# Performance work log

Measured on AMD Instinct MI355X. Metric: run time of the kernel, lower is better.

## Reference

```python
import jax, jax.numpy as jnp
import numpy as np

EPS = 1e-5

def _sage(x, src, dst, counts, w_msg, w_root, b, n_nodes):
    # mean-aggregate neighbor features (src -> dst), then linear
    msgs = x[src]                                             # [E, D]
    summed = jax.ops.segment_sum(msgs, dst, num_segments=n_nodes)
    mean = summed / counts                                    # [N, D]
    return mean @ w_msg + x @ w_root + b

def _layernorm(x, gamma, beta):
    mu = jnp.mean(x, axis=-1, keepdims=True)
    var = jnp.var(x, axis=-1, keepdims=True)
    return (x - mu) * jax.lax.rsqrt(var + EPS) * gamma + beta

def setup_inputs() -> dict:
    key = jax.random.key(0)
    N, E, D = 100000, 1600000, 128
    ks = jax.random.split(key, 20)
    z = jax.random.normal(ks[0], (N, D), dtype=jnp.float32)
    edge_index = jax.random.randint(ks[1], (2, E), 0, N, dtype=jnp.int32)
    def lin(k, din, dout):
        return jax.random.normal(k, (din, dout), dtype=jnp.float32) / np.sqrt(din)
    params = {
        'w_msg1': lin(ks[2], 128, 256), 'w_root1': lin(ks[3], 128, 256),
        'b1': jnp.zeros((256,), jnp.float32),
        'g1': jax.random.uniform(ks[4], (256,), jnp.float32, 0.9, 1.1),
        'beta1': jax.random.normal(ks[5], (256,), jnp.float32) * 0.05,
        'w_msg2': lin(ks[6], 256, 256), 'w_root2': lin(ks[7], 256, 256),
        'b2': jnp.zeros((256,), jnp.float32),
        'g2': jax.random.uniform(ks[8], (256,), jnp.float32, 0.9, 1.1),
        'beta2': jax.random.normal(ks[9], (256,), jnp.float32) * 0.05,
        'w_msg3': lin(ks[10], 256, 128), 'w_root3': lin(ks[11], 256, 128),
        'b3': jnp.zeros((128,), jnp.float32),
        'g3': jax.random.uniform(ks[12], (128,), jnp.float32, 0.9, 1.1),
        'beta3': jax.random.normal(ks[13], (128,), jnp.float32) * 0.05,
        'w_msg4': lin(ks[14], 128, 9), 'w_root4': lin(ks[15], 128, 9),
        'b4': jnp.zeros((9,), jnp.float32),
    }
    return {'z': z, 'edge_index': edge_index, **params}

def reference(z, edge_index,
              w_msg1, w_root1, b1, g1, beta1,
              w_msg2, w_root2, b2, g2, beta2,
              w_msg3, w_root3, b3, g3, beta3,
              w_msg4, w_root4, b4):
    N = z.shape[0]
    src, dst = edge_index[0], edge_index[1]
    counts = jax.ops.segment_sum(jnp.ones_like(dst, dtype=z.dtype), dst, num_segments=N)
    counts = jnp.maximum(counts, 1.0)[:, None]
    x = jax.nn.relu(_layernorm(_sage(z, src, dst, counts, w_msg1, w_root1, b1, N), g1, beta1))
    x = jax.nn.relu(_layernorm(_sage(x, src, dst, counts, w_msg2, w_root2, b2, N), g2, beta2))
    x = jax.nn.relu(_layernorm(_sage(x, src, dst, counts, w_msg3, w_root3, b3, N), g3, beta3))
    x = _sage(x, src, dst, counts, w_msg4, w_root4, b4, N)
    return x
```

## Files before the change

### kernel.cpp

```cpp
#include <hip/hip_runtime.h>
#include <hip/hip_bf16.h>


#define EPS 1e-5f

typedef unsigned short u16;
typedef short bf16x8_t __attribute__((ext_vector_type(8)));
typedef float f32x4_t __attribute__((ext_vector_type(4)));

__device__ inline unsigned int bfpack(float a, float b) {
    unsigned int ua = __builtin_bit_cast(unsigned int, a);
    unsigned int ub = __builtin_bit_cast(unsigned int, b);
    ua += 0x7fffu + ((ua >> 16) & 1u);
    ub += 0x7fffu + ((ub >> 16) & 1u);
    return (ua >> 16) | (ub & 0xffff0000u);
}

__device__ inline u16 bfr(float a) {
    unsigned int u = __builtin_bit_cast(unsigned int, a);
    u += 0x7fffu + ((u >> 16) & 1u);
    return (u16)(u >> 16);
}

__device__ inline float bf2f(u16 v) {
    unsigned int u = ((unsigned int)v) << 16;
    return __builtin_bit_cast(float, u);
}

__global__ __launch_bounds__(256) void zero_f4(float4* __restrict__ p, int n4) {
    int i = blockIdx.x * 256 + threadIdx.x;
    if (i < n4) p[i] = make_float4(0.f, 0.f, 0.f, 0.f);
}

__global__ __launch_bounds__(256) void cast_bf16(const float* __restrict__ x,
                                                 u16* __restrict__ y, int n4) {
    int i = blockIdx.x * 256 + threadIdx.x;
    if (i >= n4) return;
    float4 v = ((const float4*)x)[i];
    ((uint2*)y)[i] = make_uint2(bfpack(v.x, v.y), bfpack(v.z, v.w));
}

struct WtJobs {
    const float* W[6];
    u16* WT[6];
    int K[6], N[6];
};
__global__ __launch_bounds__(256) void transpose_cast6(WtJobs jobs) {
    int j = blockIdx.y;
    int idx = blockIdx.x * 256 + threadIdx.x;
    int K = jobs.K[j], Nn = jobs.N[j];
    if (idx >= K * Nn) return;
    int k = idx / Nn, n = idx - k * Nn;
    jobs.WT[j][(long)n * K + k] = bfr(jobs.W[j][idx]);
}

__global__ __launch_bounds__(256) void count_deg(const int* __restrict__ dst,
                                                 int* __restrict__ deg, int E) {
    int e = blockIdx.x * 256 + threadIdx.x;
    if (e < E) atomicAdd(&deg[dst[e]], 1);
}

__global__ __launch_bounds__(256) void partial_sums(const int* __restrict__ deg,
                                                    int* __restrict__ partials, int N) {
    __shared__ int lds[4];
    int tid = threadIdx.x;
    int base = blockIdx.x * 1024 + tid * 4;
    int s = 0;
    if (base + 3 < N) {
        int4 v = *(const int4*)(deg + base);
        s = v.x + v.y + v.z + v.w;
    } else {
        for (int i = 0; i < 4; ++i)
            if (base + i < N) s += deg[base + i];
    }
#pragma unroll
    for (int m = 32; m >= 1; m >>= 1) s += __shfl_xor(s, m);
    if ((tid & 63) == 0) lds[tid >> 6] = s;
    __syncthreads();
    if (tid == 0) partials[blockIdx.x] = lds[0] + lds[1] + lds[2] + lds[3];
}

__global__ __launch_bounds__(256) void scan_partials(int* __restrict__ partials, int nb) {
    __shared__ int lds[256];
    int tid = threadIdx.x;
    int v = (tid < nb) ? partials[tid] : 0;
    lds[tid] = v;
    __syncthreads();
    for (int off = 1; off < 256; off <<= 1) {
        int t = (tid >= off) ? lds[tid - off] : 0;
        __syncthreads();
        lds[tid] += t;
        __syncthreads();
    }
    if (tid < nb) partials[tid] = lds[tid] - v;
}

__global__ __launch_bounds__(256) void write_rowptr(const int* __restrict__ deg,
                                                    const int* __restrict__ partials,
                                                    int* __restrict__ rowptr,
                                                    int* __restrict__ cursor,
                                                    float* __restrict__ inv, int N, int E) {
    __shared__ int lds[256];
    int tid = threadIdx.x;
    int base = blockIdx.x * 1024 + tid * 4;
    int d[4];
    int s = 0;
#pragma unroll
    for (int i = 0; i < 4; ++i) {
        d[i] = (base + i < N) ? deg[base + i] : 0;
        s += d[i];
    }
    lds[tid] = s;
    __syncthreads();
    for (int off = 1; off < 256; off <<= 1) {
        int t = (tid >= off) ? lds[tid - off] : 0;
        __syncthreads();
        lds[tid] += t;
        __syncthreads();
    }
    int run = partials[blockIdx.x] + lds[tid] - s;
#pragma unroll
    for (int i = 0; i < 4; ++i) {
        int idx = base + i;
        if (idx < N) {
            rowptr[idx] = run;
            cursor[idx] = run;
            inv[idx] = 1.0f / fmaxf((float)d[i], 1.0f);
            run += d[i];
        }
    }
    if (blockIdx.x == 0 && tid == 0) rowptr[N] = E;
}

__global__ __launch_bounds__(256) void fill_csr_range(const int* __restrict__ src,
                                                      const int* __restrict__ dst,
                                                      int* __restrict__ cursor,
                                                      int* __restrict__ eidx, int E,
                                                      int lo, int bs) {
    int e = blockIdx.x * 256 + threadIdx.x;
    if (e >= E) return;
    int d = dst[e];
    if ((unsigned)(d - lo) < (unsigned)bs) {
        int p = atomicAdd(&cursor[d], 1);
        eidx[p] = src[e];
    }
}

__global__ __launch_bounds__(256) void gather_scale256(const u16* __restrict__ x,
                                                       const int* __restrict__ rowptr,
                                                       const int* __restrict__ eidx,
                                                       const float* __restrict__ inv,
                                                       u16* __restrict__ agg, int N) {
    int wave = threadIdx.x >> 6;
    int lane = threadIdx.x & 63;
    int row = blockIdx.x * 4 + wave;
    if (row >= N) return;
    int beg = rowptr[row], end = rowptr[row + 1];
    const ushort4* xv = (const ushort4*)x;
    float a0 = 0.f, a1 = 0.f, a2 = 0.f, a3 = 0.f;
    float c0 = 0.f, c1 = 0.f, c2 = 0.f, c3 = 0.f;
    int j = beg;
    for (; j + 1 < end; j += 2) {
        ushort4 v = xv[(long)eidx[j] * 64 + lane];
        ushort4 w = xv[(long)eidx[j + 1] * 64 + lane];
        a0 += bf2f(v.x); a1 += bf2f(v.y); a2 += bf2f(v.z); a3 += bf2f(v.w);
        c0 += bf2f(w.x); c1 += bf2f(w.y); c2 += bf2f(w.z); c3 += bf2f(w.w);
    }
    if (j < end) {
        ushort4 v = xv[(long)eidx[j] * 64 + lane];
        a0 += bf2f(v.x); a1 += bf2f(v.y); a2 += bf2f(v.z); a3 += bf2f(v.w);
    }
    float s = inv[row];
    a0 = (a0 + c0) * s; a1 = (a1 + c1) * s; a2 = (a2 + c2) * s; a3 = (a3 + c3) * s;
    ((uint2*)agg)[(long)row * 64 + lane] = make_uint2(bfpack(a0, a1), bfpack(a2, a3));
}

__global__ __launch_bounds__(256) void gather_scale128(const u16* __restrict__ x,
                                                       const int* __restrict__ rowptr,
                                                       const int* __restrict__ eidx,
                                                       const float* __restrict__ inv,
                                                       u16* __restrict__ agg, int N) {
    int half = threadIdx.x >> 5;
    int lane = threadIdx.x & 31;
    int row = blockIdx.x * 8 + half;
    if (row >= N) return;
    int beg = rowptr[row], end = rowptr[row + 1];
    const ushort4* xv = (const ushort4*)x;
    float a0 = 0.f, a1 = 0.f, a2 = 0.f, a3 = 0.f;
    float c0 = 0.f, c1 = 0.f, c2 = 0.f, c3 = 0.f;
    int j = beg;
    for (; j + 1 < end; j += 2) {
        ushort4 v = xv[(long)eidx[j] * 32 + lane];
        ushort4 w = xv[(long)eidx[j + 1] * 32 + lane];
        a0 += bf2f(v.x); a1 += bf2f(v.y); a2 += bf2f(v.z); a3 += bf2f(v.w);
        c0 += bf2f(w.x); c1 += bf2f(w.y); c2 += bf2f(w.z); c3 += bf2f(w.w);
    }
    if (j < end) {
        ushort4 v = xv[(long)eidx[j] * 32 + lane];
        a0 += bf2f(v.x); a1 += bf2f(v.y); a2 += bf2f(v.z); a3 += bf2f(v.w);
    }
    float s = inv[row];
    a0 = (a0 + c0) * s; a1 = (a1 + c1) * s; a2 = (a2 + c2) * s; a3 = (a3 + c3) * s;
    ((uint2*)agg)[(long)row * 32 + lane] = make_uint2(bfpack(a0, a1), bfpack(a2, a3));
}

__global__ __launch_bounds__(256) void gather_add_ln_relu128(const u16* __restrict__ y,
                                                             const int* __restrict__ rowptr,
                                                             const int* __restrict__ eidx,
                                                             const float* __restrict__ inv,
                                                             const u16* __restrict__ r,
                                                             const float* __restrict__ g,
                                                             const float* __restrict__ be,
                                                             u16* __restrict__ out, int N) {
    int half = threadIdx.x >> 5;
    int lane = threadIdx.x & 31;
    int row = blockIdx.x * 8 + half;
    if (row >= N) return;
    int beg = rowptr[row], end = rowptr[row + 1];
    const ushort4* xv = (const ushort4*)y;
    float a0 = 0.f, a1 = 0.f, a2 = 0.f, a3 = 0.f;
    float c0 = 0.f, c1 = 0.f, c2 = 0.f, c3 = 0.f;
    int j = beg;
    for (; j + 1 < end; j += 2) {
        ushort4 v = xv[(long)eidx[j] * 32 + lane];
        ushort4 w = xv[(long)eidx[j + 1] * 32 + lane];
        a0 += bf2f(v.x); a1 += bf2f(v.y); a2 += bf2f(v.z); a3 += bf2f(v.w);
        c0 += bf2f(w.x); c1 += bf2f(w.y); c2 += bf2f(w.z); c3 += bf2f(w.w);
    }
    if (j < end) {
        ushort4 v = xv[(long)eidx[j] * 32 + lane];
        a0 += bf2f(v.x); a1 += bf2f(v.y); a2 += bf2f(v.z); a3 += bf2f(v.w);
    }
    float iv = inv[row];
    ushort4 rr = ((const ushort4*)r)[(long)row * 32 + lane];
    float v0 = (a0 + c0) * iv + bf2f(rr.x);
    float v1 = (a1 + c1) * iv + bf2f(rr.y);
    float v2 = (a2 + c2) * iv + bf2f(rr.z);
    float v3 = (a3 + c3) * iv + bf2f(rr.w);
    float s = v0 + v1 + v2 + v3;
    float ss = v0 * v0 + v1 * v1 + v2 * v2 + v3 * v3;
#pragma unroll
    for (int m = 16; m >= 1; m >>= 1) {
        s += __shfl_xor(s, m);
        ss += __shfl_xor(ss, m);
    }
    float mean = s / 128.f;
    float var = ss / 128.f - mean * mean;
    float rs = rsqrtf(var + EPS);
    int col = lane * 4;
    v0 = fmaxf((v0 - mean) * rs * g[col + 0] + be[col + 0], 0.f);
    v1 = fmaxf((v1 - mean) * rs * g[col + 1] + be[col + 1], 0.f);
    v2 = fmaxf((v2 - mean) * rs * g[col + 2] + be[col + 2], 0.f);
    v3 = fmaxf((v3 - mean) * rs * g[col + 3] + be[col + 3], 0.f);
    ((uint2*)out)[(long)row * 32 + lane] = make_uint2(bfpack(v0, v1), bfpack(v2, v3));
}

__global__ __launch_bounds__(256) void gather9_final(const u16* __restrict__ y,
                                                     const int* __restrict__ rowptr,
                                                     const int* __restrict__ eidx,
                                                     const float* __restrict__ inv,
                                                     const float* __restrict__ r,
                                                     float* __restrict__ out, int N) {
    int idx = blockIdx.x * 256 + threadIdx.x;
    int row = idx >> 4;
    int c = idx & 15;
    if (row >= N || c >= 9) return;
    int beg = rowptr[row], end = rowptr[row + 1];
    float a = 0.f;
    for (int j = beg; j < end; ++j) a += bf2f(y[(long)eidx[j] * 9 + c]);
    out[(long)row * 9 + c] = a * inv[row] + r[(long)row * 9 + c];
}

__global__ __launch_bounds__(256) void mfma_gemm_wide_ln(const u16* A1,
                                                         const u16* __restrict__ A2,
                                                         const u16* __restrict__ WT1,
                                                         const u16* __restrict__ WT2,
                                                         const float* __restrict__ bias,
                                                         const float* __restrict__ g,
                                                         const float* __restrict__ be,
                                                         u16* out, int M, int K) {
    __shared__ __align__(16) u16 smem[64 * 260];
    u16* As = smem;
    u16* Ws = smem + 64 * 40;
    const int tid = threadIdx.x;
    const int bm = blockIdx.x * 64;
    const int l = tid & 63;
    const int w = tid >> 6;
    const int wr = (w & 1) * 32;
    const int wc = (w >> 1) * 128;
    const int ln15 = l & 15;
    const int quad = l >> 4;

    f32x4_t acc[2][8];
#pragma unroll
    for (int i = 0; i < 2; ++i)
#pragma unroll
        for (int j = 0; j < 8; ++j) acc[i][j] = (f32x4_t){0.f, 0.f, 0.f, 0.f};

    const int ar = tid >> 2;
    const int akh = (tid & 3) * 8;

    for (int pass = 0; pass < 2; ++pass) {
        const u16* A = pass ? A2 : A1;
        const u16* WT = pass ? WT2 : WT1;
        for (int k0 = 0; k0 < K; k0 += 32) {
            uint4 q0 = make_uint4(0, 0, 0, 0);
            int gr = bm + ar;
            if (gr < M) q0 = *(const uint4*)(A + (long)gr * K + k0 + akh);
            *(uint4*)(As + ar * 40 + akh) = q0;
            const u16* wp = WT + (long)tid * K + k0;
            *(uint4*)(Ws + tid * 40 + 0) = ((const uint4*)wp)[0];
            *(uint4*)(Ws + tid * 40 + 8) = ((const uint4*)wp)[1];
            *(uint4*)(Ws + tid * 40 + 16) = ((const uint4*)wp)[2];
            *(uint4*)(Ws + tid * 40 + 24) = ((const uint4*)wp)[3];
            __syncthreads();

            bf16x8_t a[2], b[8];
#pragma unroll
            for (int i = 0; i < 2; ++i)
                a[i] = *(const bf16x8_t*)(As + (wr + i * 16 + ln15) * 40 + quad * 8);
#pragma unroll
            for (int j = 0; j < 8; ++j)
                b[j] = *(const bf16x8_t*)(Ws + (wc + j * 16 + ln15) * 40 + quad * 8);
#pragma unroll
            for (int i = 0; i < 2; ++i)
#pragma unroll
                for (int j = 0; j < 8; ++j)
                    acc[i][j] = __builtin_amdgcn_mfma_f32_16x16x32_bf16(a[i], b[j], acc[i][j], 0, 0, 0);
            __syncthreads();
        }
    }

#pragma unroll
    for (int j = 0; j < 8; ++j) {
        int col = wc + j * 16 + ln15;
        float bv = bias[col];
#pragma unroll
        for (int i = 0; i < 2; ++i) {
            int row0 = wr + i * 16 + quad * 4;
            f32x4_t c = acc[i][j];
#pragma unroll
            for (int p = 0; p < 4; ++p) smem[(row0 + p) * 260 + col] = bfr(c[p] + bv);
        }
    }
    __syncthreads();

    float4 g4 = *(const float4*)&g[l * 4];
    float4 be4 = *(const float4*)&be[l * 4];
    for (int rr = 0; rr < 16; ++rr) {
        int lrow = w * 16 + rr;
        int grow = bm + lrow;
        if (grow >= M) break;
        ushort4 ld = *(const ushort4*)(smem + lrow * 260 + l * 4);
        float v0 = bf2f(ld.x), v1 = bf2f(ld.y), v2 = bf2f(ld.z), v3 = bf2f(ld.w);
        float s = v0 + v1 + v2 + v3;
        float ss = v0 * v0 + v1 * v1 + v2 * v2 + v3 * v3;
#pragma unroll
        for (int m = 32; m >= 1; m >>= 1) {
            s += __shfl_xor(s, m);
            ss += __shfl_xor(ss, m);
        }
        float mean = s / 256.f;
        float var = ss / 256.f - mean * mean;
        float rs = rsqrtf(var + EPS);
        v0 = fmaxf((v0 - mean) * rs * g4.x + be4.x, 0.f);
        v1 = fmaxf((v1 - mean) * rs * g4.y + be4.y, 0.f);
        v2 = fmaxf((v2 - mean) * rs * g4.z + be4.z, 0.f);
        v3 = fmaxf((v3 - mean) * rs * g4.w + be4.w, 0.f);
        ((uint2*)out)[(long)grow * 64 + l] = make_uint2(bfpack(v0, v1), bfpack(v2, v3));
    }
}

__global__ __launch_bounds__(256) void mfma_gemm_dual(const u16* __restrict__ A,
                                                      const u16* __restrict__ WTa,
                                                      const u16* __restrict__ WTb,
                                                      const float* __restrict__ biasb,
                                                      u16* __restrict__ outa,
                                                      u16* __restrict__ outb, int M, int K) {
    __shared__ u16 As[128 * 40];
    __shared__ u16 Ws[128 * 40];
    const u16* WT = blockIdx.y ? WTb : WTa;
    u16* out = blockIdx.y ? outb : outa;
    const float* bias = blockIdx.y ? biasb : nullptr;
    const int tid = threadIdx.x;
    const int bm = blockIdx.x * 128;
    const int l = tid & 63;
    const int w = tid >> 6;
    const int wr = (w & 1) * 64;
    const int wc = (w >> 1) * 64;
    const int ln15 = l & 15;
    const int quad = l >> 4;

    f32x4_t acc[4][4];
#pragma unroll
    for (int i = 0; i < 4; ++i)
#pragma unroll
        for (int j = 0; j < 4; ++j) acc[i][j] = (f32x4_t){0.f, 0.f, 0.f, 0.f};

    const int sr = tid >> 1;
    const int kh = (tid & 1) * 16;

    for (int k0 = 0; k0 < K; k0 += 32) {
        uint4 q0 = make_uint4(0, 0, 0, 0), q1 = make_uint4(0, 0, 0, 0);
        int gr = bm + sr;
        if (gr < M) {
            const u16* ap = A + (long)gr * K + k0 + kh;
            q0 = ((const uint4*)ap)[0];
            q1 = ((const uint4*)ap)[1];
        }
        *(uint4*)(As + sr * 40 + kh) = q0;
        *(uint4*)(As + sr * 40 + kh + 8) = q1;
        const u16* wp = WT + (long)sr * K + k0 + kh;
        *(uint4*)(Ws + sr * 40 + kh) = ((const uint4*)wp)[0];
        *(uint4*)(Ws + sr * 40 + kh + 8) = ((const uint4*)wp)[1];
        __syncthreads();

        bf16x8_t a[4], b[4];
#pragma unroll
        for (int i = 0; i < 4; ++i)
            a[i] = *(const bf16x8_t*)(As + (wr + i * 16 + ln15) * 40 + quad * 8);
#pragma unroll
        for (int j = 0; j < 4; ++j)
            b[j] = *(const bf16x8_t*)(Ws + (wc + j * 16 + ln15) * 40 + quad * 8);
#pragma unroll
        for (int i = 0; i < 4; ++i)
#pragma unroll
            for (int j = 0; j < 4; ++j)
                acc[i][j] = __builtin_amdgcn_mfma_f32_16x16x32_bf16(a[i], b[j], acc[i][j], 0, 0, 0);
        __syncthreads();
    }

#pragma unroll
    for (int j = 0; j < 4; ++j) {
        int col = wc + j * 16 + ln15;
        float bv = bias ? bias[col] : 0.f;
#pragma unroll
        for (int i = 0; i < 4; ++i) {
            int row0 = bm + wr + i * 16 + quad * 4;
            f32x4_t c = acc[i][j];
#pragma unroll
            for (int p = 0; p < 4; ++p) {
                int row = row0 + p;
                if (row < M) out[(long)row * 128 + col] = bfr(c[p] + bv);
            }
        }
    }
}

__global__ __launch_bounds__(320) void gemm4_bf(const u16* __restrict__ x,
                                                const float* __restrict__ wm,
                                                const float* __restrict__ wrt,
                                                const float* __restrict__ b,
                                                u16* __restrict__ y, float* __restrict__ r,
                                                int M) {
    __shared__ float xs[16][132];
    __shared__ float ws[128][20];
    int tid = threadIdx.x;
    int m0 = blockIdx.x * 16;
    for (int idx = tid; idx < 16 * 128; idx += 320) {
        int rr = idx >> 7, kk = idx & 127;
        int gm = m0 + rr;
        xs[rr][kk] = (gm < M) ? bf2f(x[(long)gm * 128 + kk]) : 0.f;
    }
    for (int idx = tid; idx < 128 * 18; idx += 320) {
        int kk = idx / 18, cc = idx % 18;
        ws[kk][cc] = (cc < 9) ? wm[kk * 9 + cc] : wrt[kk * 9 + cc - 9];
    }
    __syncthreads();
    if (tid < 288) {
        int rr = tid / 18, cc = tid % 18;
        float acc = 0.f;
#pragma unroll 8
        for (int kk = 0; kk < 128; ++kk) acc += xs[rr][kk] * ws[kk][cc];
        int gm = m0 + rr;
        if (gm < M) {
            if (cc < 9) y[(long)gm * 9 + cc] = bfr(acc);
            else r[(long)gm * 9 + cc - 9] = acc + b[cc - 9];
        }
    }
}

static inline int cdiv(long a, long b) { return (int)((a + b - 1) / b); }

extern "C" void kernel_launch(void* const* d_in, const int* in_sizes, int n_in,
                              void* d_out, int out_size, void* d_ws, size_t ws_size,
                              hipStream_t stream) {
    const int N = in_sizes[0] / 128;
    const int E = in_sizes[1] / 2;

    const float* z = (const float*)d_in[0];
    const int* ei = (const int*)d_in[1];
    const int* src = ei;
    const int* dstp = ei + E;
    const float* wm1 = (const float*)d_in[2];
    const float* wr1 = (const float*)d_in[3];
    const float* b1 = (const float*)d_in[4];
    const float* g1 = (const float*)d_in[5];
    const float* be1 = (const float*)d_in[6];
    const float* wm2 = (const float*)d_in[7];
    const float* wr2 = (const float*)d_in[8];
    const float* b2 = (const float*)d_in[9];
    const float* g2 = (const float*)d_in[10];
    const float* be2 = (const float*)d_in[11];
    const float* wm3 = (const float*)d_in[12];
    const float* wr3 = (const float*)d_in[13];
    const float* b3 = (const float*)d_in[14];
    const float* g3 = (const float*)d_in[15];
    const float* be3 = (const float*)d_in[16];
    const float* wm4 = (const float*)d_in[17];
    const float* wr4 = (const float*)d_in[18];
    const float* b4 = (const float*)d_in[19];
    float* out = (float*)d_out;

    u16* aggh2 = (u16*)d_ws;
    u16* h1b = aggh2 + (size_t)N * 256;
    u16* zb = h1b + (size_t)N * 256;
    u16* agg1 = zb + (size_t)N * 128;
    float* inv = (float*)(agg1 + (size_t)N * 128);
    int* deg = (int*)(inv + N);
    int* rowptr = deg + N + 4;
    int* cursor = rowptr + N + 4;
    int* partials = cursor + N + 4;
    int* eidx = partials + 256;
    u16* wt1m = (u16*)(eidx + E);
    u16* wt1r = wt1m + 256 * 128;
    u16* wt2m = wt1r + 256 * 128;
    u16* wt2r = wt2m + 256 * 256;
    u16* wt3m = wt2r + 256 * 256;
    u16* wt3r = wt3m + 128 * 256;

    u16* y3b = agg1;
    u16* r3b = zb;
    u16* h3b = h1b;
    u16* y4 = aggh2;
    float* r4 = (float*)(aggh2 + (size_t)N * 16);

    const int nscan = cdiv(N, 1024);

    cast_bf16<<<cdiv((long)N * 32, 256), 256, 0, stream>>>(z, zb, N * 32);
    zero_f4<<<cdiv(N, 1024), 256, 0, stream>>>((float4*)deg, cdiv(N, 4));
    count_deg<<<cdiv(E, 256), 256, 0, stream>>>(dstp, deg, E);
    partial_sums<<<nscan, 256, 0, stream>>>(deg, partials, N);
    scan_partials<<<1, 256, 0, stream>>>(partials, nscan);
    write_rowptr<<<nscan, 256, 0, stream>>>(deg, partials, rowptr, cursor, inv, N, E);
    {
        const int P = 8;
        int bs = cdiv(N, P);
        for (int b = 0; b < P; ++b)
            fill_csr_range<<<cdiv(E, 256), 256, 0, stream>>>(src, dstp, cursor, eidx, E,
                                                             b * bs, bs);
    }
    {
        WtJobs jobs;
        jobs.W[0] = wm1; jobs.WT[0] = wt1m; jobs.K[0] = 128; jobs.N[0] = 256;
        jobs.W[1] = wr1; jobs.WT[1] = wt1r; jobs.K[1] = 128; jobs.N[1] = 256;
        jobs.W[2] = wm2; jobs.WT[2] = wt2m; jobs.K[2] = 256; jobs.N[2] = 256;
        jobs.W[3] = wr2; jobs.WT[3] = wt2r; jobs.K[3] = 256; jobs.N[3] = 256;
        jobs.W[4] = wm3; jobs.WT[4] = wt3m; jobs.K[4] = 256; jobs.N[4] = 128;
        jobs.W[5] = wr3; jobs.WT[5] = wt3r; jobs.K[5] = 256; jobs.N[5] = 128;
        dim3 g(256, 6);
        transpose_cast6<<<g, 256, 0, stream>>>(jobs);
    }

    gather_scale128<<<cdiv(N, 8), 256, 0, stream>>>(zb, rowptr, eidx, inv, agg1, N);
    mfma_gemm_wide_ln<<<cdiv(N, 64), 256, 0, stream>>>(agg1, zb, wt1m, wt1r, b1, g1, be1,
                                                       h1b, N, 128);

    gather_scale256<<<cdiv(N, 4), 256, 0, stream>>>(h1b, rowptr, eidx, inv, aggh2, N);
    mfma_gemm_wide_ln<<<cdiv(N, 64), 256, 0, stream>>>(aggh2, h1b, wt2m, wt2r, b2, g2, be2,
                                                       aggh2, N, 256);

    {
        dim3 g(cdiv(N, 128), 2);
        mfma_gemm_dual<<<g, 256, 0, stream>>>(aggh2, wt3m, wt3r, b3, y3b, r3b, N, 256);
    }
    gather_add_ln_relu128<<<cdiv(N, 8), 256, 0, stream>>>(y3b, rowptr, eidx, inv, r3b, g3,
                                                          be3, h3b, N);

    gemm4_bf<<<cdiv(N, 16), 320, 0, stream>>>(h3b, wm4, wr4, b4, y4, r4, N);
    gather9_final<<<cdiv((long)N * 16, 256), 256, 0, stream>>>(y4, rowptr, eidx, inv, r4, out, N);
}
```

Baseline: 861.9 us.

## Split edges across wave sub-groups with 16-byte gathers and shuffle reduction

```diff
diff --git a/kernel.cpp b/kernel.cpp
--- a/kernel.cpp
+++ b/kernel.cpp
@@ -26,6 +26,15 @@
     unsigned int u = ((unsigned int)v) << 16;
     return __builtin_bit_cast(float, u);
 }
+
+__device__ inline float bflo(unsigned int q) { return __builtin_bit_cast(float, q << 16); }
+__device__ inline float bfhi(unsigned int q) { return __builtin_bit_cast(float, q & 0xffff0000u); }
+
+#define ACC8(A, Q)                                         \
+    A[0] += bflo(Q.x); A[1] += bfhi(Q.x);                  \
+    A[2] += bflo(Q.y); A[3] += bfhi(Q.y);                  \
+    A[4] += bflo(Q.z); A[5] += bfhi(Q.z);                  \
+    A[6] += bflo(Q.w); A[7] += bfhi(Q.w);
 
 __global__ __launch_bounds__(256) void zero_f4(float4* __restrict__ p, int n4) {
     int i = blockIdx.x * 256 + threadIdx.x;
@@ -153,26 +162,37 @@
                                                        u16* __restrict__ agg, int N) {
     int wave = threadIdx.x >> 6;
     int lane = threadIdx.x & 63;
+    int half = lane >> 5;
+    int sub = lane & 31;
     int row = blockIdx.x * 4 + wave;
     if (row >= N) return;
     int beg = rowptr[row], end = rowptr[row + 1];
-    const ushort4* xv = (const ushort4*)x;
-    float a0 = 0.f, a1 = 0.f, a2 = 0.f, a3 = 0.f;
-    float c0 = 0.f, c1 = 0.f, c2 = 0.f, c3 = 0.f;
-    int j = beg;
-    for (; j + 1 < end; j += 2) {
-        ushort4 v = xv[(long)eidx[j] * 64 + lane];
-        ushort4 w = xv[(long)eidx[j + 1] * 64 + lane];
-        a0 += bf2f(v.x); a1 += bf2f(v.y); a2 += bf2f(v.z); a3 += bf2f(v.w);
-        c0 += bf2f(w.x); c1 += bf2f(w.y); c2 += bf2f(w.z); c3 += bf2f(w.w);
+    float a[8] = {}, b[8] = {};
+    int j = beg + half;
+    for (; j + 2 < end; j += 4) {
+        uint4 q0 = *(const uint4*)(x + (long)eidx[j] * 256 + sub * 8);
+        uint4 q1 = *(const uint4*)(x + (long)eidx[j + 2] * 256 + sub * 8);
+        ACC8(a, q0);
+        ACC8(b, q1);
     }
     if (j < end) {
-        ushort4 v = xv[(long)eidx[j] * 64 + lane];
-        a0 += bf2f(v.x); a1 += bf2f(v.y); a2 += bf2f(v.z); a3 += bf2f(v.w);
-    }
-    float s = inv[row];
-    a0 = (a0 + c0) * s; a1 = (a1 + c1) * s; a2 = (a2 + c2) * s; a3 = (a3 + c3) * s;
-    ((uint2*)agg)[(long)row * 64 + lane] = make_uint2(bfpack(a0, a1), bfpack(a2, a3));
+        uint4 q = *(const uint4*)(x + (long)eidx[j] * 256 + sub * 8);
+        ACC8(a, q);
+    }
+#pragma unroll
+    for (int i = 0; i < 8; ++i) {
+        a[i] += b[i];
+        a[i] += __shfl_xor(a[i], 32);
+    }
+    if (half == 0) {
+        float s = inv[row];
+        uint4 o;
+        o.x = bfpack(a[0] * s, a[1] * s);
+        o.y = bfpack(a[2] * s, a[3] * s);
+        o.z = bfpack(a[4] * s, a[5] * s);
+        o.w = bfpack(a[6] * s, a[7] * s);
+        *(uint4*)(agg + (long)row * 256 + sub * 8) = o;
+    }
 }
 
 __global__ __launch_bounds__(256) void gather_scale128(const u16* __restrict__ x,
@@ -180,28 +200,40 @@
                                                        const int* __restrict__ eidx,
                                                        const float* __restrict__ inv,
                                                        u16* __restrict__ agg, int N) {
-    int half = threadIdx.x >> 5;
-    int lane = threadIdx.x & 31;
-    int row = blockIdx.x * 8 + half;
+    int wave = threadIdx.x >> 6;
+    int lane = threadIdx.x & 63;
+    int quarter = lane >> 4;
+    int sub = lane & 15;
+    int row = blockIdx.x * 4 + wave;
     if (row >= N) return;
     int beg = rowptr[row], end = rowptr[row + 1];
-    const ushort4* xv = (const ushort4*)x;
-    float a0 = 0.f, a1 = 0.f, a2 = 0.f, a3 = 0.f;
-    float c0 = 0.f, c1 = 0.f, c2 = 0.f, c3 = 0.f;
-    int j = beg;
-    for (; j + 1 < end; j += 2) {
-        ushort4 v = xv[(long)eidx[j] * 32 + lane];
-        ushort4 w = xv[(long)eidx[j + 1] * 32 + lane];
-        a0 += bf2f(v.x); a1 += bf2f(v.y); a2 += bf2f(v.z); a3 += bf2f(v.w);
-        c0 += bf2f(w.x); c1 += bf2f(w.y); c2 += bf2f(w.z); c3 += bf2f(w.w);
+    float a[8] = {}, b[8] = {};
+    int j = beg + quarter;
+    for (; j + 4 < end; j += 8) {
+        uint4 q0 = *(const uint4*)(x + (long)eidx[j] * 128 + sub * 8);
+        uint4 q1 = *(const uint4*)(x + (long)eidx[j + 4] * 128 + sub * 8);
+        ACC8(a, q0);
+        ACC8(b, q1);
     }
     if (j < end) {
-        ushort4 v = xv[(long)eidx[j] * 32 + lane];
-        a0 += bf2f(v.x); a1 += bf2f(v.y); a2 += bf2f(v.z); a3 += bf2f(v.w);
-    }
-    float s = inv[row];
-    a0 = (a0 + c0) * s; a1 = (a1 + c1) * s; a2 = (a2 + c2) * s; a3 = (a3 + c3) * s;
-    ((uint2*)agg)[(long)row * 32 + lane] = make_uint2(bfpack(a0, a1), bfpack(a2, a3));
+        uint4 q = *(const uint4*)(x + (long)eidx[j] * 128 + sub * 8);
+        ACC8(a, q);
+    }
+#pragma unroll
+    for (int i = 0; i < 8; ++i) {
+        a[i] += b[i];
+        a[i] += __shfl_xor(a[i], 16);
+        a[i] += __shfl_xor(a[i], 32);
+    }
+    if (quarter == 0) {
+        float s = inv[row];
+        uint4 o;
+        o.x = bfpack(a[0] * s, a[1] * s);
+        o.y = bfpack(a[2] * s, a[3] * s);
+        o.z = bfpack(a[4] * s, a[5] * s);
+        o.w = bfpack(a[6] * s, a[7] * s);
+        *(uint4*)(agg + (long)row * 128 + sub * 8) = o;
+    }
 }
 
 __global__ __launch_bounds__(256) void gather_add_ln_relu128(const u16* __restrict__ y,
@@ -212,47 +244,70 @@
                                                              const float* __restrict__ g,
                                                              const float* __restrict__ be,
                                                              u16* __restrict__ out, int N) {
-    int half = threadIdx.x >> 5;
-    int lane = threadIdx.x & 31;
-    int row = blockIdx.x * 8 + half;
+    int wave = threadIdx.x >> 6;
+    int lane = threadIdx.x & 63;
+    int quarter = lane >> 4;
+    int sub = lane & 15;
+    int row = blockIdx.x * 4 + wave;
     if (row >= N) return;
     int beg = rowptr[row], end = rowptr[row + 1];
-    const ushort4* xv = (const ushort4*)y;
-    float a0 = 0.f, a1 = 0.f, a2 = 0.f, a3 = 0.f;
-    float c0 = 0.f, c1 = 0.f, c2 = 0.f, c3 = 0.f;
-    int j = beg;
-    for (; j + 1 < end; j += 2) {
-        ushort4 v = xv[(long)eidx[j] * 32 + lane];
-        ushort4 w = xv[(long)eidx[j + 1] * 32 + lane];
-        a0 += bf2f(v.x); a1 += bf2f(v.y); a2 += bf2f(v.z); a3 += bf2f(v.w);
-        c0 += bf2f(w.x); c1 += bf2f(w.y); c2 += bf2f(w.z); c3 += bf2f(w.w);
+    float a[8] = {}, b[8] = {};
+    int j = beg + quarter;
+    for (; j + 4 < end; j += 8) {
+        uint4 q0 = *(const uint4*)(y + (long)eidx[j] * 128 + sub * 8);
+        uint4 q1 = *(const uint4*)(y + (long)eidx[j + 4] * 128 + sub * 8);
+        ACC8(a, q0);
+        ACC8(b, q1);
     }
     if (j < end) {
-        ushort4 v = xv[(long)eidx[j] * 32 + lane];
-        a0 += bf2f(v.x); a1 += bf2f(v.y); a2 += bf2f(v.z); a3 += bf2f(v.w);
+        uint4 q = *(const uint4*)(y + (long)eidx[j] * 128 + sub * 8);
+        ACC8(a, q);
+    }
+#pragma unroll
+    for (int i = 0; i < 8; ++i) {
+        a[i] += b[i];
+        a[i] += __shfl_xor(a[i], 16);
+        a[i] += __shfl_xor(a[i], 32);
     }
     float iv = inv[row];
-    ushort4 rr = ((const ushort4*)r)[(long)row * 32 + lane];
-    float v0 = (a0 + c0) * iv + bf2f(rr.x);
-    float v1 = (a1 + c1) * iv + bf2f(rr.y);
-    float v2 = (a2 + c2) * iv + bf2f(rr.z);
-    float v3 = (a3 + c3) * iv + bf2f(rr.w);
-    float s = v0 + v1 + v2 + v3;
-    float ss = v0 * v0 + v1 * v1 + v2 * v2 + v3 * v3;
-#pragma unroll
-    for (int m = 16; m >= 1; m >>= 1) {
+    uint4 rr = *(const uint4*)(r + (long)row * 128 + sub * 8);
+    float v[8];
+    v[0] = a[0] * iv + bflo(rr.x); v[1] = a[1] * iv + bfhi(rr.x);
+    v[2] = a[2] * iv + bflo(rr.y); v[3] = a[3] * iv + bfhi(rr.y);
+    v[4] = a[4] * iv + bflo(rr.z); v[5] = a[5] * iv + bfhi(rr.z);
+    v[6] = a[6] * iv + bflo(rr.w); v[7] = a[7] * iv + bfhi(rr.w);
+    float s = 0.f, ss = 0.f;
+#pragma unroll
+    for (int i = 0; i < 8; ++i) { s += v[i]; ss += v[i] * v[i]; }
+#pragma unroll
+    for (int m = 8; m >= 1; m >>= 1) {
         s += __shfl_xor(s, m);
         ss += __shfl_xor(ss, m);
     }
     float mean = s / 128.f;
     float var = ss / 128.f - mean * mean;
     float rs = rsqrtf(var + EPS);
-    int col = lane * 4;
-    v0 = fmaxf((v0 - mean) * rs * g[col + 0] + be[col + 0], 0.f);
-    v1 = fmaxf((v1 - mean) * rs * g[col + 1] + be[col + 1], 0.f);
-    v2 = fmaxf((v2 - mean) * rs * g[col + 2] + be[col + 2], 0.f);
-    v3 = fmaxf((v3 - mean) * rs * g[col + 3] + be[col + 3], 0.f);
-    ((uint2*)out)[(long)row * 32 + lane] = make_uint2(bfpack(v0, v1), bfpack(v2, v3));
+    if (quarter == 0) {
+        int col = sub * 8;
+        float4 g0 = *(const float4*)&g[col];
+        float4 g1 = *(const float4*)&g[col + 4];
+        float4 e0 = *(const float4*)&be[col];
+        float4 e1 = *(const float4*)&be[col + 4];
+        float o0 = fmaxf((v[0] - mean) * rs * g0.x + e0.x, 0.f);
+        float o1 = fmaxf((v[1] - mean) * rs * g0.y + e0.y, 0.f);
+        float o2 = fmaxf((v[2] - mean) * rs * g0.z + e0.z, 0.f);
+        float o3 = fmaxf((v[3] - mean) * rs * g0.w + e0.w, 0.f);
+        float o4 = fmaxf((v[4] - mean) * rs * g1.x + e1.x, 0.f);
+        float o5 = fmaxf((v[5] - mean) * rs * g1.y + e1.y, 0.f);
+        float o6 = fmaxf((v[6] - mean) * rs * g1.z + e1.z, 0.f);
+        float o7 = fmaxf((v[7] - mean) * rs * g1.w + e1.w, 0.f);
+        uint4 o;
+        o.x = bfpack(o0, o1);
+        o.y = bfpack(o2, o3);
+        o.z = bfpack(o4, o5);
+        o.w = bfpack(o6, o7);
+        *(uint4*)(out + (long)row * 128 + sub * 8) = o;
+    }
 }
 
 __global__ __launch_bounds__(256) void gather9_final(const u16* __restrict__ y,
@@ -544,7 +599,7 @@
     scan_partials<<<1, 256, 0, stream>>>(partials, nscan);
     write_rowptr<<<nscan, 256, 0, stream>>>(deg, partials, rowptr, cursor, inv, N, E);
     {
-        const int P = 8;
+        const int P = 4;
         int bs = cdiv(N, P);
         for (int b = 0; b < P; ++b)
             fill_csr_range<<<cdiv(E, 256), 256, 0, stream>>>(src, dstp, cursor, eidx, E,
@@ -562,7 +617,7 @@
         transpose_cast6<<<g, 256, 0, stream>>>(jobs);
     }
 
-    gather_scale128<<<cdiv(N, 8), 256, 0, stream>>>(zb, rowptr, eidx, inv, agg1, N);
+    gather_scale128<<<cdiv(N, 4), 256, 0, stream>>>(zb, rowptr, eidx, inv, agg1, N);
     mfma_gemm_wide_ln<<<cdiv(N, 64), 256, 0, stream>>>(agg1, zb, wt1m, wt1r, b1, g1, be1,
                                                        h1b, N, 128);
 
@@ -574,7 +629,7 @@
         dim3 g(cdiv(N, 128), 2);
         mfma_gemm_dual<<<g, 256, 0, stream>>>(aggh2, wt3m, wt3r, b3, y3b, r3b, N, 256);
     }
-    gather_add_ln_relu128<<<cdiv(N, 8), 256, 0, stream>>>(y3b, rowptr, eidx, inv, r3b, g3,
+    gather_add_ln_relu128<<<cdiv(N, 4), 256, 0, stream>>>(y3b, rowptr, eidx, inv, r3b, g3,
                                                           be3, h3b, N);
 
     gemm4_bf<<<cdiv(N, 16), 320, 0, stream>>>(h3b, wm4, wr4, b4, y4, r4, N);
```

Result: faster. 829.8 us (-3.7%).
